# Kernel optimization log

Measured on AMD Instinct MI355X. Metric: run time of the kernel, lower is better.

Reference implementation:

```python
import jax, jax.numpy as jnp
import numpy as np

B, S, ENC, DEC, ATT = 32, 2048, 1024, 1024, 1024


def setup_inputs() -> dict:
    key = jax.random.key(0)
    k1, k2, k3, k4, k5, k6 = jax.random.split(key, 6)
    sc = lambda fan_in: 1.0 / np.sqrt(fan_in)
    return {
        "encoder_hidden_states": jax.random.normal(k1, (B, S, ENC), dtype=jnp.float32),
        "decoder_hidden_state": jax.random.normal(k2, (B, 1, DEC), dtype=jnp.float32),
        # nn.Linear stores weight as [out, in]; we keep [in, out] for x @ W
        "U_a": jax.random.uniform(k3, (ENC, ATT), jnp.float32, -sc(ENC), sc(ENC)),
        "W_a": jax.random.uniform(k4, (DEC, ATT), jnp.float32, -sc(DEC), sc(DEC)),
        "v_t": jax.random.uniform(k5, (ATT, 1), jnp.float32, -sc(ATT), sc(ATT)),
        "ffn": jax.random.uniform(k6, (ENC + DEC, DEC), jnp.float32, -sc(ENC + DEC), sc(ENC + DEC)),
    }


def reference(encoder_hidden_states, decoder_hidden_state, U_a, W_a, v_t, ffn):
    # additive (Bahdanau) attention
    u = jnp.einsum('bse,ea->bsa', encoder_hidden_states, U_a)      # [B,S,A]
    w = jnp.einsum('bqd,da->bqa', decoder_hidden_state, W_a)       # [B,1,A]
    e = jnp.tanh(w + u) @ v_t                                      # [B,S,1]
    align = jax.nn.softmax(e, axis=1)                              # softmax over seq
    # context = alignment^T @ encoder_states  -> [B,1,E]
    context = jnp.einsum('bsq,bse->bqe', align, encoder_hidden_states)
    cat = jnp.concatenate([decoder_hidden_state, context], axis=-1)  # [B,1,D+E]
    output = jnp.tanh(cat @ ffn)                                     # [B,1,D]
    return (output, context)
```

## Files before the change

kernel.cpp:

```cpp
#include <hip/hip_runtime.h>
#include <hip/hip_bf16.h>
#include <cstdint>
#include <cstddef>

#define B_  32
#define S_  2048
#define E_  1024
#define A_  1024
#define D_  1024
#define M_TOT (B_ * S_)

typedef __attribute__((ext_vector_type(8))) __bf16 bf16x8;
typedef __attribute__((ext_vector_type(4))) float  f32x4;

__device__ __forceinline__ float fast_tanh(float x) {
    float cx = fminf(fmaxf(x, -15.f), 15.f);
    float e2 = __expf(2.f * cx);
    return 1.f - 2.f / (e2 + 1.f);
}

__device__ __forceinline__ bf16x8 pack8(float4 f0, float4 f1) {
    bf16x8 r;
    r[0] = (__bf16)f0.x; r[1] = (__bf16)f0.y; r[2] = (__bf16)f0.z; r[3] = (__bf16)f0.w;
    r[4] = (__bf16)f1.x; r[5] = (__bf16)f1.y; r[6] = (__bf16)f1.z; r[7] = (__bf16)f1.w;
    return r;
}

typedef __attribute__((address_space(3))) uint32_t lds_u32_t;
typedef __attribute__((address_space(1))) const uint32_t gbl_u32_t;
__device__ __forceinline__ void async_ld16(const void* g, void* l) {
    __builtin_amdgcn_global_load_lds((gbl_u32_t*)g,
                                     (lds_u32_t*)(uint32_t)(uintptr_t)l,
                                     16, 0, 0);
}

__global__ __launch_bounds__(256) void k_trans_U(const float* __restrict__ Ua,
                                                 __bf16* __restrict__ Ut) {
    __shared__ float tile[64][65];
    int bid = blockIdx.x;
    int k0 = (bid >> 4) * 64, n0 = (bid & 15) * 64;
    int t = threadIdx.x;
    int r = t >> 6, c = t & 63;
    #pragma unroll
    for (int i = 0; i < 16; ++i)
        tile[i * 4 + r][c] = Ua[(size_t)(k0 + i * 4 + r) * 1024 + n0 + c];
    __syncthreads();
    #pragma unroll
    for (int i = 0; i < 16; ++i)
        Ut[(size_t)(n0 + i * 4 + r) * 1024 + k0 + c] = (__bf16)tile[c][i * 4 + r];
}

__global__ __launch_bounds__(256) void k_w_part(const float* __restrict__ dec,
                                                const float* __restrict__ Wa,
                                                float* __restrict__ w_part) {
    int bid = blockIdx.x;
    int ac = bid & 3, b = (bid >> 2) & 31, kc = bid >> 7;
    int a = ac * 256 + threadIdx.x;
    int k0 = kc * 128;
    float acc = 0.f;
    #pragma unroll 8
    for (int k = 0; k < 128; ++k)
        acc += dec[b * 1024 + k0 + k] * Wa[(size_t)(k0 + k) * 1024 + a];
    w_part[kc * 32768 + b * 1024 + a] = acc;
}

__global__ __launch_bounds__(256) void k_gemm_e(
        const float* __restrict__ enc, const __bf16* __restrict__ Ut,
        const float* __restrict__ w_part, const float* __restrict__ v,
        float* __restrict__ e_part) {
    __shared__ __bf16 lX[2][128 * 32];
    __shared__ __bf16 lU[2][128 * 32];
    __shared__ float  e_lds[2][128];

    const int t = threadIdx.x;
    const int bid = blockIdx.x;
    const int xcd = bid & 7;
    const int j_  = bid >> 3;
    const int m_tile = xcd * 64 + (j_ >> 3);
    const int n_tile = j_ & 7;
    const int m0 = m_tile * 128;
    const int n0 = n_tile * 128;
    const int wave = t >> 6;
    const int lane = t & 63;
    const int q = lane >> 4;
    const int c = lane & 15;
    const int wm = (wave >> 1) * 64;
    const int wn = (wave & 1) * 64;

    f32x4 acc[4][4];
    #pragma unroll
    for (int i = 0; i < 4; ++i)
        #pragma unroll
        for (int j = 0; j < 4; ++j)
            #pragma unroll
            for (int r = 0; r < 4; ++r) acc[i][j][r] = 0.f;

    const int lrow = lane >> 2;
    const int lcol = (lane & 3) * 8;
    const int xrow = wave * 32;

    const float*  gxa = enc + (size_t)(m0 + xrow + lrow) * 1024 + lcol;
    const __bf16* gub = Ut  + (size_t)(n0 + xrow + lrow) * 1024 + lcol;

    float4 f0, f1, f2, f3;
    auto loadA = [&](int kk) {
        const float* p = gxa + kk;
        f0 = *(const float4*)p;
        f1 = *(const float4*)(p + 4);
        f2 = *(const float4*)(p + 16 * 1024);
        f3 = *(const float4*)(p + 16 * 1024 + 4);
    };
    auto writeA = [&](int bsel) {
        *(bf16x8*)(&lX[bsel][(xrow + lrow) * 32 + lcol])      = pack8(f0, f1);
        *(bf16x8*)(&lX[bsel][(xrow + 16 + lrow) * 32 + lcol]) = pack8(f2, f3);
    };
    auto stageB = [&](int kk, int bsel) {
        async_ld16(gub + kk,             &lU[bsel][xrow * 32]);
        async_ld16(gub + kk + 16 * 1024, &lU[bsel][(xrow + 16) * 32]);
    };
    auto compute = [&](int bsel) {
        bf16x8 af[4], bfr[4];
        #pragma unroll
        for (int i = 0; i < 4; ++i)
            af[i] = *(const bf16x8*)(&lX[bsel][(wm + i * 16 + c) * 32 + q * 8]);
        #pragma unroll
        for (int j = 0; j < 4; ++j)
            bfr[j] = *(const bf16x8*)(&lU[bsel][(wn + j * 16 + c) * 32 + q * 8]);
        #pragma unroll
        for (int i = 0; i < 4; ++i)
            #pragma unroll
            for (int j = 0; j < 4; ++j)
                acc[i][j] = __builtin_amdgcn_mfma_f32_16x16x32_bf16(af[i], bfr[j], acc[i][j], 0, 0, 0);
    };

    loadA(0);
    stageB(0, 0);
    writeA(0);
    __syncthreads();

    for (int kk = 0; kk < 1024; kk += 64) {
        if (kk + 32 < 1024) { loadA(kk + 32); stageB(kk + 32, 1); }
        compute(0);
        if (kk + 32 < 1024) writeA(1);
        __syncthreads();
        if (kk + 64 < 1024) { loadA(kk + 64); stageB(kk + 64, 0); }
        compute(1);
        if (kk + 64 < 1024) writeA(0);
        __syncthreads();
    }

    const int b_idx = m0 >> 11;
    float wv[4], vv[4];
    #pragma unroll
    for (int j = 0; j < 4; ++j) {
        int col = n0 + wn + j * 16 + c;
        float s = 0.f;
        #pragma unroll
        for (int p = 0; p < 8; ++p) s += w_part[p * 32768 + b_idx * 1024 + col];
        wv[j] = s;
        vv[j] = v[col];
    }
    #pragma unroll
    for (int i = 0; i < 4; ++i) {
        float s0 = 0.f, s1 = 0.f, s2 = 0.f, s3 = 0.f;
        #pragma unroll
        for (int j = 0; j < 4; ++j) {
            s0 += fast_tanh(wv[j] + acc[i][j][0]) * vv[j];
            s1 += fast_tanh(wv[j] + acc[i][j][1]) * vv[j];
            s2 += fast_tanh(wv[j] + acc[i][j][2]) * vv[j];
            s3 += fast_tanh(wv[j] + acc[i][j][3]) * vv[j];
        }
        #pragma unroll
        for (int off = 1; off < 16; off <<= 1) {
            s0 += __shfl_xor(s0, off, 16);
            s1 += __shfl_xor(s1, off, 16);
            s2 += __shfl_xor(s2, off, 16);
            s3 += __shfl_xor(s3, off, 16);
        }
        if (c == 0) {
            int row = wm + i * 16 + q * 4;
            e_lds[wave & 1][row + 0] = s0;
            e_lds[wave & 1][row + 1] = s1;
            e_lds[wave & 1][row + 2] = s2;
            e_lds[wave & 1][row + 3] = s3;
        }
    }
    __syncthreads();
    if (t < 128)
        e_part[(size_t)n_tile * M_TOT + m0 + t] = e_lds[0][t] + e_lds[1][t];
}

__global__ __launch_bounds__(256) void k_softmax(const float* __restrict__ ep,
                                                 float* __restrict__ al) {
    int b = blockIdx.x, t = threadIdx.x;
    float ev[8];
    #pragma unroll
    for (int i = 0; i < 8; ++i) {
        int s = i * 256 + t;
        float x = 0.f;
        #pragma unroll
        for (int p = 0; p < 8; ++p) x += ep[p * M_TOT + b * 2048 + s];
        ev[i] = x;
    }
    float mx = ev[0];
    #pragma unroll
    for (int i = 1; i < 8; ++i) mx = fmaxf(mx, ev[i]);
    #pragma unroll
    for (int off = 1; off < 64; off <<= 1) mx = fmaxf(mx, __shfl_xor(mx, off, 64));
    __shared__ float redm[4];
    if ((t & 63) == 0) redm[t >> 6] = mx;
    __syncthreads();
    mx = fmaxf(fmaxf(redm[0], redm[1]), fmaxf(redm[2], redm[3]));

    float ex[8], sm = 0.f;
    #pragma unroll
    for (int i = 0; i < 8; ++i) { ex[i] = __expf(ev[i] - mx); sm += ex[i]; }
    #pragma unroll
    for (int off = 1; off < 64; off <<= 1) sm += __shfl_xor(sm, off, 64);
    __shared__ float reds[4];
    if ((t & 63) == 0) reds[t >> 6] = sm;
    __syncthreads();
    sm = reds[0] + reds[1] + reds[2] + reds[3];
    float inv = 1.f / sm;
    #pragma unroll
    for (int i = 0; i < 8; ++i) al[b * 2048 + i * 256 + t] = ex[i] * inv;
}

__global__ __launch_bounds__(256) void k_ctx(const float* __restrict__ enc,
                                             const float* __restrict__ al,
                                             float* __restrict__ ctx_part) {
    int b  = blockIdx.x >> 5;
    int sc = blockIdx.x & 31;
    int t  = threadIdx.x;
    int e4 = t * 4;
    float ax = 0.f, ay = 0.f, az = 0.f, aw = 0.f;
    int sbase = sc * 64;
    for (int i = 0; i < 64; i += 4) {
        #pragma unroll
        for (int u = 0; u < 4; ++u) {
            int s = sbase + i + u;
            float a = al[b * 2048 + s];
            float4 x = *(const float4*)(enc + (size_t)(b * 2048 + s) * 1024 + e4);
            ax += a * x.x; ay += a * x.y; az += a * x.z; aw += a * x.w;
        }
    }
    float4 r; r.x = ax; r.y = ay; r.z = az; r.w = aw;
    *(float4*)(ctx_part + ((size_t)sc * 32 + b) * 1024 + e4) = r;
}

__global__ __launch_bounds__(256) void k_final(const float* __restrict__ dec,
                                               const float* __restrict__ ffn,
                                               const float* __restrict__ ctx_part,
                                               float* __restrict__ out) {
    int b  = blockIdx.x >> 4;
    int dc = blockIdx.x & 15;
    int t  = threadIdx.x;
    __shared__ float cat[2048];
    __shared__ float red[4][64];

    #pragma unroll
    for (int r = 0; r < 4; ++r) {
        int e = r * 256 + t;
        cat[e] = dec[b * 1024 + e];
        float s = 0.f;
        #pragma unroll
        for (int p = 0; p < 32; ++p) s += ctx_part[((size_t)p * 32 + b) * 1024 + e];
        cat[1024 + e] = s;
        if (dc == 0) out[32768 + b * 1024 + e] = s;
    }
    __syncthreads();

    int dl = t & 63, ic = t >> 6;
    int d  = dc * 64 + dl;
    float acc = 0.f;
    int i0 = ic * 512;
    for (int i = 0; i < 512; i += 4) {
        float4 cv = *(const float4*)(cat + i0 + i);
        const float* fr = ffn + (size_t)(i0 + i) * 1024 + d;
        acc += cv.x * fr[0];
        acc += cv.y * fr[1024];
        acc += cv.z * fr[2048];
        acc += cv.w * fr[3072];
    }
    red[ic][dl] = acc;
    __syncthreads();
    if (t < 64) {
        float s = red[0][t] + red[1][t] + red[2][t] + red[3][t];
        out[b * 1024 + dc * 64 + t] = fast_tanh(s);
    }
}

extern "C" void kernel_launch(void* const* d_in, const int* in_sizes, int n_in,
                              void* d_out, int out_size, void* d_ws, size_t ws_size,
                              hipStream_t stream) {
    const float* enc = (const float*)d_in[0];
    const float* dec = (const float*)d_in[1];
    const float* Ua  = (const float*)d_in[2];
    const float* Wa  = (const float*)d_in[3];
    const float* vt  = (const float*)d_in[4];
    const float* ffn = (const float*)d_in[5];
    float* out = (float*)d_out;

    char* ws = (char*)d_ws;
    size_t off = 0;
    __bf16* Ut       = (__bf16*)(ws + off); off += (size_t)A_ * E_ * 2;
    float*  e_part   = (float*)(ws + off);  off += (size_t)8 * M_TOT * 4;
    float*  al       = (float*)(ws + off);  off += (size_t)M_TOT * 4;
    float*  w_part   = (float*)(ws + off);  off += (size_t)8 * B_ * 1024 * 4;
    float*  ctx_part = (float*)(ws + off);  off += (size_t)32 * B_ * 1024 * 4;

    k_trans_U<<<256, 256, 0, stream>>>(Ua, Ut);
    k_w_part<<<1024, 256, 0, stream>>>(dec, Wa, w_part);
    k_gemm_e<<<4096, 256, 0, stream>>>(enc, Ut, w_part, vt, e_part);
    k_softmax<<<B_, 256, 0, stream>>>(e_part, al);
    k_ctx<<<B_ * 32, 256, 0, stream>>>(enc, al, ctx_part);
    k_final<<<B_ * 16, 256, 0, stream>>>(dec, ffn, ctx_part, out);
}
```

Baseline: 698.5 us.

## Pre-convert encoder states to bf16 and stream A tiles asynchronously into LDS

A new kernel converts the whole fp32 encoder tensor to bf16 in workspace. The GEMM then loads its A tiles with global_load_lds direct-to-LDS copies instead of loading fp32 into registers, converting, and storing to LDS. The LDS column layout of both operands is XOR-swizzled to avoid bank conflicts on the fragment reads. This takes conversion and VGPR staging off the GEMM's critical path, at the cost of an extra full pass over the encoder (a 256MB read plus a 128MB write) and a larger workspace requirement; when the workspace is too small, the kernel falls back to the old path.

```diff
diff --git a/kernel.cpp b/kernel.cpp
--- a/kernel.cpp
+++ b/kernel.cpp
@@ -32,6 +32,18 @@
     __builtin_amdgcn_global_load_lds((gbl_u32_t*)g,
                                      (lds_u32_t*)(uint32_t)(uintptr_t)l,
                                      16, 0, 0);
+}
+
+__global__ __launch_bounds__(256) void k_cvt(const float* __restrict__ enc,
+                                             __bf16* __restrict__ encB) {
+    size_t base = (size_t)blockIdx.x * 8192 + (size_t)threadIdx.x * 8;
+    #pragma unroll
+    for (int it = 0; it < 4; ++it) {
+        size_t idx = base + (size_t)it * 2048;
+        float4 f0 = *(const float4*)(enc + idx);
+        float4 f1 = *(const float4*)(enc + idx + 4);
+        *(bf16x8*)(encB + idx) = pack8(f0, f1);
+    }
 }
 
 __global__ __launch_bounds__(256) void k_trans_U(const float* __restrict__ Ua,
@@ -64,8 +76,10 @@
     w_part[kc * 32768 + b * 1024 + a] = acc;
 }
 
+template<bool ASYNC_A>
 __global__ __launch_bounds__(256) void k_gemm_e(
-        const float* __restrict__ enc, const __bf16* __restrict__ Ut,
+        const float* __restrict__ enc, const __bf16* __restrict__ encB,
+        const __bf16* __restrict__ Ut,
         const float* __restrict__ w_part, const float* __restrict__ v,
         float* __restrict__ e_part) {
     __shared__ __bf16 lX[2][128 * 32];
@@ -96,36 +110,46 @@
             for (int r = 0; r < 4; ++r) acc[i][j][r] = 0.f;
 
     const int lrow = lane >> 2;
-    const int lcol = (lane & 3) * 8;
+    const int p    = lane & 3;
+    const int sw   = (lrow >> 1) & 3;
+    const int lcolS = ((p ^ sw)) * 8;
+
     const int xrow = wave * 32;
 
-    const float*  gxa = enc + (size_t)(m0 + xrow + lrow) * 1024 + lcol;
-    const __bf16* gub = Ut  + (size_t)(n0 + xrow + lrow) * 1024 + lcol;
+    const float*  gxa = enc  + (size_t)(m0 + xrow + lrow) * 1024 + lcolS;
+    const __bf16* gxb = encB + (size_t)(m0 + xrow + lrow) * 1024 + lcolS;
+    const __bf16* gub = Ut   + (size_t)(n0 + xrow + lrow) * 1024 + lcolS;
 
     float4 f0, f1, f2, f3;
     auto loadA = [&](int kk) {
-        const float* p = gxa + kk;
-        f0 = *(const float4*)p;
-        f1 = *(const float4*)(p + 4);
-        f2 = *(const float4*)(p + 16 * 1024);
-        f3 = *(const float4*)(p + 16 * 1024 + 4);
+        const float* pp = gxa + kk;
+        f0 = *(const float4*)pp;
+        f1 = *(const float4*)(pp + 4);
+        f2 = *(const float4*)(pp + 16 * 1024);
+        f3 = *(const float4*)(pp + 16 * 1024 + 4);
     };
     auto writeA = [&](int bsel) {
-        *(bf16x8*)(&lX[bsel][(xrow + lrow) * 32 + lcol])      = pack8(f0, f1);
-        *(bf16x8*)(&lX[bsel][(xrow + 16 + lrow) * 32 + lcol]) = pack8(f2, f3);
+        *(bf16x8*)(&lX[bsel][(xrow + lrow) * 32 + p * 8])      = pack8(f0, f1);
+        *(bf16x8*)(&lX[bsel][(xrow + 16 + lrow) * 32 + p * 8]) = pack8(f2, f3);
+    };
+    auto stageA = [&](int kk, int bsel) {
+        async_ld16(gxb + kk,             &lX[bsel][xrow * 32]);
+        async_ld16(gxb + kk + 16 * 1024, &lX[bsel][(xrow + 16) * 32]);
     };
     auto stageB = [&](int kk, int bsel) {
         async_ld16(gub + kk,             &lU[bsel][xrow * 32]);
         async_ld16(gub + kk + 16 * 1024, &lU[bsel][(xrow + 16) * 32]);
     };
+
+    const int fcol = (q ^ ((c >> 1) & 3)) * 8;
     auto compute = [&](int bsel) {
         bf16x8 af[4], bfr[4];
         #pragma unroll
         for (int i = 0; i < 4; ++i)
-            af[i] = *(const bf16x8*)(&lX[bsel][(wm + i * 16 + c) * 32 + q * 8]);
+            af[i] = *(const bf16x8*)(&lX[bsel][(wm + i * 16 + c) * 32 + fcol]);
         #pragma unroll
         for (int j = 0; j < 4; ++j)
-            bfr[j] = *(const bf16x8*)(&lU[bsel][(wn + j * 16 + c) * 32 + q * 8]);
+            bfr[j] = *(const bf16x8*)(&lU[bsel][(wn + j * 16 + c) * 32 + fcol]);
         #pragma unroll
         for (int i = 0; i < 4; ++i)
             #pragma unroll
@@ -133,20 +157,32 @@
                 acc[i][j] = __builtin_amdgcn_mfma_f32_16x16x32_bf16(af[i], bfr[j], acc[i][j], 0, 0, 0);
     };
 
-    loadA(0);
-    stageB(0, 0);
-    writeA(0);
-    __syncthreads();
-
-    for (int kk = 0; kk < 1024; kk += 64) {
-        if (kk + 32 < 1024) { loadA(kk + 32); stageB(kk + 32, 1); }
-        compute(0);
-        if (kk + 32 < 1024) writeA(1);
+    if constexpr (ASYNC_A) {
+        stageA(0, 0); stageB(0, 0);
         __syncthreads();
-        if (kk + 64 < 1024) { loadA(kk + 64); stageB(kk + 64, 0); }
-        compute(1);
-        if (kk + 64 < 1024) writeA(0);
+        for (int kk = 0; kk < 1024; kk += 64) {
+            if (kk + 32 < 1024) { stageA(kk + 32, 1); stageB(kk + 32, 1); }
+            compute(0);
+            __syncthreads();
+            if (kk + 64 < 1024) { stageA(kk + 64, 0); stageB(kk + 64, 0); }
+            compute(1);
+            __syncthreads();
+        }
+    } else {
+        loadA(0);
+        stageB(0, 0);
+        writeA(0);
         __syncthreads();
+        for (int kk = 0; kk < 1024; kk += 64) {
+            if (kk + 32 < 1024) { loadA(kk + 32); stageB(kk + 32, 1); }
+            compute(0);
+            if (kk + 32 < 1024) writeA(1);
+            __syncthreads();
+            if (kk + 64 < 1024) { loadA(kk + 64); stageB(kk + 64, 0); }
+            compute(1);
+            if (kk + 64 < 1024) writeA(0);
+            __syncthreads();
+        }
     }
 
     const int b_idx = m0 >> 11;
@@ -156,7 +192,7 @@
         int col = n0 + wn + j * 16 + c;
         float s = 0.f;
         #pragma unroll
-        for (int p = 0; p < 8; ++p) s += w_part[p * 32768 + b_idx * 1024 + col];
+        for (int pp = 0; pp < 8; ++pp) s += w_part[pp * 32768 + b_idx * 1024 + col];
         wv[j] = s;
         vv[j] = v[col];
     }
@@ -308,10 +344,17 @@
     float*  al       = (float*)(ws + off);  off += (size_t)M_TOT * 4;
     float*  w_part   = (float*)(ws + off);  off += (size_t)8 * B_ * 1024 * 4;
     float*  ctx_part = (float*)(ws + off);  off += (size_t)32 * B_ * 1024 * 4;
+    __bf16* encB     = (__bf16*)(ws + off); off += (size_t)M_TOT * E_ * 2;
+    const bool use_async = ws_size >= off;
 
     k_trans_U<<<256, 256, 0, stream>>>(Ua, Ut);
     k_w_part<<<1024, 256, 0, stream>>>(dec, Wa, w_part);
-    k_gemm_e<<<4096, 256, 0, stream>>>(enc, Ut, w_part, vt, e_part);
+    if (use_async) {
+        k_cvt<<<8192, 256, 0, stream>>>(enc, encB);
+        k_gemm_e<true><<<4096, 256, 0, stream>>>(enc, encB, Ut, w_part, vt, e_part);
+    } else {
+        k_gemm_e<false><<<4096, 256, 0, stream>>>(enc, encB, Ut, w_part, vt, e_part);
+    }
     k_softmax<<<B_, 256, 0, stream>>>(e_part, al);
     k_ctx<<<B_ * 32, 256, 0, stream>>>(enc, al, ctx_part);
     k_final<<<B_ * 16, 256, 0, stream>>>(dec, ffn, ctx_part, out);
```

After: 696.9 us. About the same (-0.2%).
